# Performance work log

Measured on AMD Instinct MI355X. Metric: run time of the kernel, lower is better.

The kernel has to match this reference:

```python
import math
import jax, jax.numpy as jnp
import numpy as np

B = 64
INPUT_SIZE = 10080
PATCH = 18
S = INPUT_SIZE // PATCH  # 560 patches
E = 96                    # embed_dim
H = 12                    # num_heads
D = 96                    # head_dim == embed_dim (PAT quirk)
F = 256                   # ff_dim
L = 2                     # num_layers
EPS = 1e-5


def _sinusoidal_pe(seq_len, embed_dim):
    pos = jnp.arange(seq_len, dtype=jnp.float32)[:, None]
    div = jnp.exp(jnp.arange(0, embed_dim, 2, dtype=jnp.float32) * (-math.log(10000.0) / embed_dim))
    pe = jnp.zeros((seq_len, embed_dim), dtype=jnp.float32)
    pe = pe.at[:, 0::2].set(jnp.sin(pos * div))
    pe = pe.at[:, 1::2].set(jnp.cos(pos * div))
    return pe


def _layernorm(x, g, b):
    mu = jnp.mean(x, axis=-1, keepdims=True)
    var = jnp.var(x, axis=-1, keepdims=True)
    return (x - mu) * jax.lax.rsqrt(var + EPS) * g + b


def setup_inputs() -> dict:
    key = jax.random.key(0)
    ks = jax.random.split(key, 12)
    sd = 0.02
    inp = {
        "x": jax.random.normal(ks[0], (B, INPUT_SIZE), dtype=jnp.float32),
        "patch_W": jax.random.normal(ks[1], (PATCH, E), dtype=jnp.float32) * sd,
        "patch_b": jnp.zeros((E,), jnp.float32),
        "Wq": jax.random.normal(ks[2], (L, H, E, D), dtype=jnp.float32) * sd,
        "bq": jnp.zeros((L, H, D), jnp.float32),
        "Wk": jax.random.normal(ks[3], (L, H, E, D), dtype=jnp.float32) * sd,
        "bk": jnp.zeros((L, H, D), jnp.float32),
        "Wv": jax.random.normal(ks[4], (L, H, E, D), dtype=jnp.float32) * sd,
        "bv": jnp.zeros((L, H, D), jnp.float32),
        "Wo": jax.random.normal(ks[5], (L, H * D, E), dtype=jnp.float32) * sd,
        "bo": jnp.zeros((L, E), jnp.float32),
        "ff1_W": jax.random.normal(ks[6], (L, E, F), dtype=jnp.float32) * sd,
        "ff1_b": jnp.zeros((L, F), jnp.float32),
        "ff2_W": jax.random.normal(ks[7], (L, F, E), dtype=jnp.float32) * sd,
        "ff2_b": jnp.zeros((L, E), jnp.float32),
        "n1_g": jnp.ones((L, E), jnp.float32),
        "n1_b": jnp.zeros((L, E), jnp.float32),
        "n2_g": jnp.ones((L, E), jnp.float32),
        "n2_b": jnp.zeros((L, E), jnp.float32),
    }
    return inp


def reference(x, patch_W, patch_b, Wq, bq, Wk, bk, Wv, bv, Wo, bo,
              ff1_W, ff1_b, ff2_W, ff2_b, n1_g, n1_b, n2_g, n2_b):
    scale = 1.0 / math.sqrt(D)
    # patch embedding: [B, S, PATCH] -> [B, S, E]
    h = x.reshape(B, S, PATCH) @ patch_W + patch_b
    h = h + _sinusoidal_pe(S, E)[None]
    for l in range(L):
        # all heads at once (original loops over heads; same math)
        q = jnp.einsum('bse,hed->bhsd', h, Wq[l]) + bq[l][None, :, None, :]
        k = jnp.einsum('bse,hed->bhsd', h, Wk[l]) + bk[l][None, :, None, :]
        v = jnp.einsum('bse,hed->bhsd', h, Wv[l]) + bv[l][None, :, None, :]
        scores = jnp.einsum('bhsd,bhtd->bhst', q, k) * scale
        attn = jax.nn.softmax(scores, axis=-1)
        heads = jnp.einsum('bhst,bhtd->bhsd', attn, v)
        concat = heads.transpose(0, 2, 1, 3).reshape(B, S, H * D)
        attn_out = concat @ Wo[l] + bo[l]
        h = _layernorm(h + attn_out, n1_g[l], n1_b[l])
        ff = jax.nn.relu(h @ ff1_W[l] + ff1_b[l]) @ ff2_W[l] + ff2_b[l]
        h = _layernorm(h + ff, n2_g[l], n2_b[l])
    return h
```

## Files before the change

kernel.cpp:

```cpp
#include <hip/hip_runtime.h>
#include <hip/hip_bf16.h>
#include <math.h>

#define BATCH 64
#define CHUNK 32
#define INPUT_SIZE 10080
#define PATCH 18
#define SEQ 560
#define EMB 96
#define NHEAD 12
#define HDIM 96
#define FFDIM 256
#define NLAYER 2
#define TOK (BATCH * SEQ)
#define EPSV 1e-5f
#define SCALE 0.10206207261596577f

typedef __attribute__((ext_vector_type(8))) short bf16x8;
typedef __attribute__((ext_vector_type(4))) short bf16x4;
typedef __attribute__((ext_vector_type(4))) float f32x4;

static __device__ __forceinline__ short f2bf(float x) {
  union { __hip_bfloat16 b; short s; } u;
  u.b = __float2bfloat16(x);
  return u.s;
}

__global__ __launch_bounds__(256) void allprep_kernel(
    const float* __restrict__ Wq, const float* __restrict__ Wk,
    const float* __restrict__ Wv, const float* __restrict__ Wo,
    const float* __restrict__ ff1_W, const float* __restrict__ ff2_W,
    __hip_bfloat16* __restrict__ wqT, __hip_bfloat16* __restrict__ wkvT,
    __hip_bfloat16* __restrict__ woT, __hip_bfloat16* __restrict__ ff1WT,
    __hip_bfloat16* __restrict__ ff2WT) {
  int bx = blockIdx.x;
  if (bx < 72) {
    int hh = bx % NHEAD, mat = (bx / NHEAD) % 3, l = bx / 36;
    const float* src = (mat == 0 ? Wq : (mat == 1 ? Wk : Wv)) +
                       ((size_t)l * NHEAD + hh) * EMB * HDIM;
    __shared__ float t[HDIM * 97];
    for (int i = threadIdx.x; i < EMB * HDIM; i += 256) {
      int e = i / HDIM, d = i % HDIM;
      t[d * 97 + e] = src[i];
    }
    __syncthreads();
    __hip_bfloat16* dst;
    if (mat == 0)
      dst = wqT + ((size_t)l * NHEAD + hh) * HDIM * EMB;
    else
      dst = wkvT + ((size_t)l * 2 * NHEAD * HDIM + (mat - 1) * NHEAD * HDIM +
                    hh * HDIM) * EMB;
    for (int j = threadIdx.x; j < HDIM * EMB; j += 256) {
      int d = j / EMB, e = j % EMB;
      dst[j] = __float2bfloat16(t[d * 97 + e]);
    }
  } else if (bx < 74) {
    int l = bx - 72;
    const float* src = Wo + (size_t)l * NHEAD * HDIM * EMB;
    __hip_bfloat16* dst = woT + (size_t)l * EMB * NHEAD * HDIM;
    for (int i = threadIdx.x; i < EMB * NHEAD * HDIM; i += 256) {
      int e = i / (NHEAD * HDIM), j = i % (NHEAD * HDIM);
      dst[i] = __float2bfloat16(src[(size_t)j * EMB + e]);
    }
  } else {
    int idx = bx - 74;
    int mat = idx % 2, l = idx / 2;
    if (mat == 0) {
      const float* src = ff1_W + (size_t)l * EMB * FFDIM;
      __hip_bfloat16* dst = ff1WT + (size_t)l * FFDIM * EMB;
      for (int i = threadIdx.x; i < FFDIM * EMB; i += 256) {
        int f = i / EMB, e = i % EMB;
        dst[i] = __float2bfloat16(src[(size_t)e * FFDIM + f]);
      }
    } else {
      const float* src = ff2_W + (size_t)l * FFDIM * EMB;
      __hip_bfloat16* dst = ff2WT + (size_t)l * EMB * FFDIM;
      for (int i = threadIdx.x; i < EMB * FFDIM; i += 256) {
        int e = i / FFDIM, f = i % FFDIM;
        dst[i] = __float2bfloat16(src[(size_t)f * EMB + e]);
      }
    }
  }
}

__global__ void patch_pe_kernel(const float* __restrict__ x,
                                const float* __restrict__ W,
                                const float* __restrict__ bias,
                                float* __restrict__ h,
                                __hip_bfloat16* __restrict__ hbf) {
  int gid = blockIdx.x * blockDim.x + threadIdx.x;
  if (gid >= TOK * EMB) return;
  int tok = gid / EMB;
  int e = gid % EMB;
  int b = tok / SEQ;
  int s = tok % SEQ;
  const float* xp = x + b * INPUT_SIZE + s * PATCH;
  float acc = bias[e];
#pragma unroll
  for (int p = 0; p < PATCH; p++) acc += xp[p] * W[p * EMB + e];
  int i = e >> 1;
  float freq = __expf(-(float)(2 * i) * (9.210340371976184f / 96.0f));
  float ang = (float)s * freq;
  acc += (e & 1) ? cosf(ang) : sinf(ang);
  h[gid] = acc;
  hbf[gid] = __float2bfloat16(acc);
}

__global__ __launch_bounds__(256) void kv_mfma_kernel(
    const __hip_bfloat16* __restrict__ hbf,
    const __hip_bfloat16* __restrict__ wkvT, const float* __restrict__ bk,
    const float* __restrict__ bv, __hip_bfloat16* __restrict__ kbuf,
    __hip_bfloat16* __restrict__ vbufT, int b0) {
  const int wave = threadIdx.x >> 6;
  const int lane = threadIdx.x & 63;
  const int tq = lane & 15;
  const int quad = lane >> 4;
  const int m0 = blockIdx.x * 64 + wave * 16;
  const int n0 = blockIdx.y * 64;

  __shared__ short tile[4][16][68];

  const short* ap =
      (const short*)hbf + ((size_t)b0 * SEQ + m0 + tq) * EMB + quad * 8;
  bf16x8 a0 = *(const bf16x8*)(ap);
  bf16x8 a1 = *(const bf16x8*)(ap + 32);
  bf16x8 a2 = *(const bf16x8*)(ap + 64);

  f32x4 acc[4];
  const f32x4 zero4 = {0.f, 0.f, 0.f, 0.f};
#pragma unroll
  for (int nt = 0; nt < 4; nt++) acc[nt] = zero4;
#pragma unroll
  for (int nt = 0; nt < 4; nt++) {
    const short* bp =
        (const short*)wkvT + (size_t)(n0 + nt * 16 + tq) * EMB + quad * 8;
    bf16x8 b0f = *(const bf16x8*)(bp);
    bf16x8 b1f = *(const bf16x8*)(bp + 32);
    bf16x8 b2f = *(const bf16x8*)(bp + 64);
    acc[nt] = __builtin_amdgcn_mfma_f32_16x16x32_bf16(a0, b0f, acc[nt], 0, 0, 0);
    acc[nt] = __builtin_amdgcn_mfma_f32_16x16x32_bf16(a1, b1f, acc[nt], 0, 0, 0);
    acc[nt] = __builtin_amdgcn_mfma_f32_16x16x32_bf16(a2, b2f, acc[nt], 0, 0, 0);
  }

  const int tl0 = m0 + quad * 4;
  const int blb = tl0 / SEQ;
  const int ss0 = tl0 - blb * SEQ;

  if (n0 < NHEAD * HDIM) {
#pragma unroll
    for (int nt = 0; nt < 4; nt++) {
      int n = n0 + nt * 16 + tq;
      float bias = bk[n];
#pragma unroll
      for (int j = 0; j < 4; j++)
        tile[wave][quad * 4 + j][nt * 16 + tq] = f2bf(acc[nt][j] + bias);
    }
#pragma unroll
    for (int it = 0; it < 2; it++) {
      int idx = it * 64 + lane;
      int row = idx >> 3;
      int seg = idx & 7;
      int tl = m0 + row;
      int bb = tl / SEQ;
      int ss = tl - bb * SEQ;
      int r0s = n0 + seg * 8;
      int hh2 = r0s / HDIM;
      int d0 = r0s - hh2 * HDIM;
      bf16x8 v = *(const bf16x8*)&tile[wave][row][seg * 8];
      *(bf16x8*)((short*)kbuf +
                 ((size_t)(bb * NHEAD + hh2) * SEQ + ss) * HDIM + d0) = v;
    }
  } else {
#pragma unroll
    for (int nt = 0; nt < 4; nt++) {
      int n = n0 + nt * 16 + tq;
      int r = n - NHEAD * HDIM;
      int hh2 = r / HDIM;
      int d = r - hh2 * HDIM;
      float bias = bv[r];
      bf16x4 pack;
#pragma unroll
      for (int j = 0; j < 4; j++) pack[j] = f2bf(acc[nt][j] + bias);
      *(bf16x4*)((short*)vbufT +
                 ((size_t)(blb * NHEAD + hh2) * HDIM + d) * SEQ + ss0) = pack;
    }
  }
}

#define QW 104
#define PW 72
__global__ __launch_bounds__(256, 3) void attn_flash_kernel(
    const __hip_bfloat16* __restrict__ hbf,
    const __hip_bfloat16* __restrict__ wqT, const float* __restrict__ bq,
    const __hip_bfloat16* __restrict__ kbuf,
    const __hip_bfloat16* __restrict__ vbufT,
    __hip_bfloat16* __restrict__ heads, int b0) {
  const int flat = blockIdx.x;
  const int xcd = flat & 7;
  const int slot = flat >> 3;
  const int g = (slot / 5) * 8 + xcd;
  const int qt = slot % 5;
  const int hh = g % NHEAD;
  const int bl = g / NHEAD;
  const int wave = threadIdx.x >> 6;
  const int lane = threadIdx.x & 63;
  const int tq = lane & 15;
  const int quad = lane >> 4;

  __shared__ __align__(16) short sbuf[4][3328];
  short* pw = sbuf[wave];

  const size_t bh = (size_t)(bl * NHEAD + hh);
  const short* kb = (const short*)kbuf + bh * SEQ * HDIM;
  const short* vb = (const short*)vbufT + bh * HDIM * SEQ;

  const int q0 = qt * 128 + wave * 32;

  int qrA = q0 + tq;      if (qrA > SEQ - 1) qrA = SEQ - 1;
  int qrB = q0 + 16 + tq; if (qrB > SEQ - 1) qrB = SEQ - 1;
  const short* hpA =
      (const short*)hbf + ((size_t)(b0 + bl) * SEQ + qrA) * EMB + quad * 8;
  const short* hpB =
      (const short*)hbf + ((size_t)(b0 + bl) * SEQ + qrB) * EMB + quad * 8;
  bf16x8 haA0 = *(const bf16x8*)(hpA);
  bf16x8 haA1 = *(const bf16x8*)(hpA + 32);
  bf16x8 haA2 = *(const bf16x8*)(hpA + 64);
  bf16x8 haB0 = *(const bf16x8*)(hpB);
  bf16x8 haB1 = *(const bf16x8*)(hpB + 32);
  bf16x8 haB2 = *(const bf16x8*)(hpB + 64);
  const f32x4 zero4 = {0.f, 0.f, 0.f, 0.f};
  f32x4 qaccA[6], qaccB[6];
#pragma unroll
  for (int dt = 0; dt < 6; dt++) { qaccA[dt] = zero4; qaccB[dt] = zero4; }
#pragma unroll
  for (int dt = 0; dt < 6; dt++) {
    const short* wp = (const short*)wqT +
                      ((size_t)hh * HDIM + dt * 16 + tq) * EMB + quad * 8;
    bf16x8 w0 = *(const bf16x8*)(wp);
    bf16x8 w1 = *(const bf16x8*)(wp + 32);
    bf16x8 w2 = *(const bf16x8*)(wp + 64);
    qaccA[dt] = __builtin_amdgcn_mfma_f32_16x16x32_bf16(haA0, w0, qaccA[dt], 0, 0, 0);
    qaccA[dt] = __builtin_amdgcn_mfma_f32_16x16x32_bf16(haA1, w1, qaccA[dt], 0, 0, 0);
    qaccA[dt] = __builtin_amdgcn_mfma_f32_16x16x32_bf16(haA2, w2, qaccA[dt], 0, 0, 0);
    qaccB[dt] = __builtin_amdgcn_mfma_f32_16x16x32_bf16(haB0, w0, qaccB[dt], 0, 0, 0);
    qaccB[dt] = __builtin_amdgcn_mfma_f32_16x16x32_bf16(haB1, w1, qaccB[dt], 0, 0, 0);
    qaccB[dt] = __builtin_amdgcn_mfma_f32_16x16x32_bf16(haB2, w2, qaccB[dt], 0, 0, 0);
  }
#pragma unroll
  for (int dt = 0; dt < 6; dt++) {
    int d = dt * 16 + tq;
    float bias = bq[hh * HDIM + d];
#pragma unroll
    for (int r = 0; r < 4; r++) {
      pw[(quad * 4 + r) * QW + d] = f2bf((qaccA[dt][r] + bias) * SCALE);
      pw[(16 + quad * 4 + r) * QW + d] = f2bf((qaccB[dt][r] + bias) * SCALE);
    }
  }
  bf16x8 aqA0 = *(const bf16x8*)&pw[tq * QW + quad * 8];
  bf16x8 aqA1 = *(const bf16x8*)&pw[tq * QW + 32 + quad * 8];
  bf16x8 aqA2 = *(const bf16x8*)&pw[tq * QW + 64 + quad * 8];
  bf16x8 aqB0 = *(const bf16x8*)&pw[(16 + tq) * QW + quad * 8];
  bf16x8 aqB1 = *(const bf16x8*)&pw[(16 + tq) * QW + 32 + quad * 8];
  bf16x8 aqB2 = *(const bf16x8*)&pw[(16 + tq) * QW + 64 + quad * 8];

  f32x4 oA[6], oB[6];
#pragma unroll
  for (int dt = 0; dt < 6; dt++) { oA[dt] = zero4; oB[dt] = zero4; }
  float mA[4], mB[4], lA[4], lB[4];
#pragma unroll
  for (int r = 0; r < 4; r++) {
    mA[r] = -1e30f; mB[r] = -1e30f; lA[r] = 0.f; lB[r] = 0.f;
  }

  for (int c = 0; c < 9; c++) {
    const int col0 = c * 64;
    f32x4 sA[4], sB[4];
#pragma unroll
    for (int t = 0; t < 4; t++) { sA[t] = zero4; sB[t] = zero4; }
#pragma unroll
    for (int t = 0; t < 4; t++) {
      const short* kp = kb + (size_t)(col0 + t * 16 + tq) * HDIM + quad * 8;
      bf16x8 k0 = *(const bf16x8*)(kp);
      bf16x8 k1 = *(const bf16x8*)(kp + 32);
      bf16x8 k2 = *(const bf16x8*)(kp + 64);
      sA[t] = __builtin_amdgcn_mfma_f32_16x16x32_bf16(aqA0, k0, sA[t], 0, 0, 0);
      sA[t] = __builtin_amdgcn_mfma_f32_16x16x32_bf16(aqA1, k1, sA[t], 0, 0, 0);
      sA[t] = __builtin_amdgcn_mfma_f32_16x16x32_bf16(aqA2, k2, sA[t], 0, 0, 0);
      sB[t] = __builtin_amdgcn_mfma_f32_16x16x32_bf16(aqB0, k0, sB[t], 0, 0, 0);
      sB[t] = __builtin_amdgcn_mfma_f32_16x16x32_bf16(aqB1, k1, sB[t], 0, 0, 0);
      sB[t] = __builtin_amdgcn_mfma_f32_16x16x32_bf16(aqB2, k2, sB[t], 0, 0, 0);
    }
    if (c == 8) {
#pragma unroll
      for (int r = 0; r < 4; r++) { sA[3][r] = -1e30f; sB[3][r] = -1e30f; }
    }
    float cA[4], cB[4];
#pragma unroll
    for (int r = 0; r < 4; r++) {
      cA[r] = fmaxf(fmaxf(sA[0][r], sA[1][r]), fmaxf(sA[2][r], sA[3][r]));
      cB[r] = fmaxf(fmaxf(sB[0][r], sB[1][r]), fmaxf(sB[2][r], sB[3][r]));
    }
#pragma unroll
    for (int mask = 1; mask < 16; mask <<= 1) {
#pragma unroll
      for (int r = 0; r < 4; r++) {
        cA[r] = fmaxf(cA[r], __shfl_xor(cA[r], mask, 64));
        cB[r] = fmaxf(cB[r], __shfl_xor(cB[r], mask, 64));
      }
    }
    bool need = false;
#pragma unroll
    for (int r = 0; r < 4; r++)
      need = need | (cA[r] > mA[r]) | (cB[r] > mB[r]);
    if (__any(need)) {
#pragma unroll
      for (int r = 0; r < 4; r++) {
        float mnA = fmaxf(mA[r], cA[r]);
        float fA = __expf(mA[r] - mnA);
        mA[r] = mnA; lA[r] *= fA;
        float mnB = fmaxf(mB[r], cB[r]);
        float fB = __expf(mB[r] - mnB);
        mB[r] = mnB; lB[r] *= fB;
#pragma unroll
        for (int dt = 0; dt < 6; dt++) { oA[dt][r] *= fA; oB[dt][r] *= fB; }
      }
    }
#pragma unroll
    for (int t = 0; t < 4; t++) {
#pragma unroll
      for (int r = 0; r < 4; r++) {
        float pA = __expf(sA[t][r] - mA[r]);
        lA[r] += pA;
        pw[(quad * 4 + r) * PW + t * 16 + tq] = f2bf(pA);
        float pB = __expf(sB[t][r] - mB[r]);
        lB[r] += pB;
        pw[(16 + quad * 4 + r) * PW + t * 16 + tq] = f2bf(pB);
      }
    }
    bf16x8 paA0 = *(const bf16x8*)&pw[tq * PW + quad * 8];
    bf16x8 paA1 = *(const bf16x8*)&pw[tq * PW + 32 + quad * 8];
    bf16x8 paB0 = *(const bf16x8*)&pw[(16 + tq) * PW + quad * 8];
    bf16x8 paB1 = *(const bf16x8*)&pw[(16 + tq) * PW + 32 + quad * 8];
#pragma unroll
    for (int dt = 0; dt < 6; dt++) {
      const short* vp = vb + (size_t)(dt * 16 + tq) * SEQ + col0 + quad * 8;
      bf16x8 v0 = *(const bf16x8*)(vp);
      bf16x8 v1 = *(const bf16x8*)(vp + 32);
      oA[dt] = __builtin_amdgcn_mfma_f32_16x16x32_bf16(paA0, v0, oA[dt], 0, 0, 0);
      oA[dt] = __builtin_amdgcn_mfma_f32_16x16x32_bf16(paA1, v1, oA[dt], 0, 0, 0);
      oB[dt] = __builtin_amdgcn_mfma_f32_16x16x32_bf16(paB0, v0, oB[dt], 0, 0, 0);
      oB[dt] = __builtin_amdgcn_mfma_f32_16x16x32_bf16(paB1, v1, oB[dt], 0, 0, 0);
    }
  }

#pragma unroll
  for (int mask = 1; mask < 16; mask <<= 1) {
#pragma unroll
    for (int r = 0; r < 4; r++) {
      lA[r] += __shfl_xor(lA[r], mask, 64);
      lB[r] += __shfl_xor(lB[r], mask, 64);
    }
  }
  float rA[4], rB[4];
#pragma unroll
  for (int r = 0; r < 4; r++) { rA[r] = 1.f / lA[r]; rB[r] = 1.f / lB[r]; }
  __hip_bfloat16* hpout =
      heads + ((size_t)(b0 + bl) * SEQ) * (NHEAD * HDIM) + (size_t)hh * HDIM;
  const int qgA = q0 + quad * 4;
  const int qgB = q0 + 16 + quad * 4;
#pragma unroll
  for (int dt = 0; dt < 6; dt++) {
    int d = dt * 16 + tq;
#pragma unroll
    for (int r = 0; r < 4; r++) {
      if (qgA + r < SEQ)
        hpout[(size_t)(qgA + r) * (NHEAD * HDIM) + d] =
            __float2bfloat16(oA[dt][r] * rA[r]);
      if (qgB + r < SEQ)
        hpout[(size_t)(qgB + r) * (NHEAD * HDIM) + d] =
            __float2bfloat16(oB[dt][r] * rB[r]);
    }
  }
}

__global__ __launch_bounds__(256) void wo_ln_mfma_kernel(
    const __hip_bfloat16* __restrict__ heads,
    const __hip_bfloat16* __restrict__ woT, const float* __restrict__ bo,
    const float* __restrict__ gamma, const float* __restrict__ beta,
    const float* __restrict__ hres, float* __restrict__ hA,
    __hip_bfloat16* __restrict__ hbf) {
  const int wave = threadIdx.x >> 6;
  const int lane = threadIdx.x & 63;
  const int tq = lane & 15;
  const int quad = lane >> 4;
  const int m0 = blockIdx.x * 64 + wave * 16;

  const short* ap = (const short*)heads + (size_t)(m0 + tq) * (NHEAD * HDIM);
  const short* bp = (const short*)woT;

  f32x4 acc[6];
  const f32x4 zero4 = {0.f, 0.f, 0.f, 0.f};
#pragma unroll
  for (int dt = 0; dt < 6; dt++) acc[dt] = zero4;

  for (int kt = 0; kt < 36; kt++) {
    bf16x8 af = *(const bf16x8*)(ap + kt * 32 + quad * 8);
#pragma unroll
    for (int dt = 0; dt < 6; dt++) {
      bf16x8 bfr = *(const bf16x8*)(bp + (size_t)(dt * 16 + tq) * (NHEAD * HDIM) +
                                    kt * 32 + quad * 8);
      acc[dt] = __builtin_amdgcn_mfma_f32_16x16x32_bf16(af, bfr, acc[dt], 0, 0, 0);
    }
  }

  const int tok0 = m0 + quad * 4;
  float s1[4] = {0.f, 0.f, 0.f, 0.f};
  float s2[4] = {0.f, 0.f, 0.f, 0.f};
#pragma unroll
  for (int dt = 0; dt < 6; dt++) {
    int n = dt * 16 + tq;
    float bias = bo[n];
#pragma unroll
    for (int r = 0; r < 4; r++) {
      float val = acc[dt][r] + bias + hres[(size_t)(tok0 + r) * EMB + n];
      acc[dt][r] = val;
      s1[r] += val;
      s2[r] += val * val;
    }
  }
#pragma unroll
  for (int mask = 1; mask < 16; mask <<= 1) {
#pragma unroll
    for (int r = 0; r < 4; r++) {
      s1[r] += __shfl_xor(s1[r], mask, 64);
      s2[r] += __shfl_xor(s2[r], mask, 64);
    }
  }
  float mean[4], rstd[4];
#pragma unroll
  for (int r = 0; r < 4; r++) {
    mean[r] = s1[r] * (1.0f / EMB);
    float var = s2[r] * (1.0f / EMB) - mean[r] * mean[r];
    rstd[r] = rsqrtf(var + EPSV);
  }
#pragma unroll
  for (int dt = 0; dt < 6; dt++) {
    int n = dt * 16 + tq;
    float g = gamma[n], bt = beta[n];
#pragma unroll
    for (int r = 0; r < 4; r++) {
      float o = (acc[dt][r] - mean[r]) * rstd[r] * g + bt;
      hA[(size_t)(tok0 + r) * EMB + n] = o;
      hbf[(size_t)(tok0 + r) * EMB + n] = __float2bfloat16(o);
    }
  }
}

__global__ __launch_bounds__(256) void ff1_mfma_kernel(
    const __hip_bfloat16* __restrict__ hbf,
    const __hip_bfloat16* __restrict__ ff1WT, const float* __restrict__ b1,
    __hip_bfloat16* __restrict__ ffbf) {
  const int wave = threadIdx.x >> 6;
  const int lane = threadIdx.x & 63;
  const int tq = lane & 15;
  const int quad = lane >> 4;
  const int m0 = blockIdx.x * 64 + wave * 16;

  const short* ap = (const short*)hbf + (size_t)(m0 + tq) * EMB + quad * 8;
  bf16x8 a0 = *(const bf16x8*)(ap);
  bf16x8 a1 = *(const bf16x8*)(ap + 32);
  bf16x8 a2 = *(const bf16x8*)(ap + 64);

  f32x4 acc[16];
  const f32x4 zero4 = {0.f, 0.f, 0.f, 0.f};
#pragma unroll
  for (int nt = 0; nt < 16; nt++) acc[nt] = zero4;
#pragma unroll
  for (int nt = 0; nt < 16; nt++) {
    const short* bp =
        (const short*)ff1WT + (size_t)(nt * 16 + tq) * EMB + quad * 8;
    bf16x8 b0f = *(const bf16x8*)(bp);
    bf16x8 b1f = *(const bf16x8*)(bp + 32);
    bf16x8 b2f = *(const bf16x8*)(bp + 64);
    acc[nt] = __builtin_amdgcn_mfma_f32_16x16x32_bf16(a0, b0f, acc[nt], 0, 0, 0);
    acc[nt] = __builtin_amdgcn_mfma_f32_16x16x32_bf16(a1, b1f, acc[nt], 0, 0, 0);
    acc[nt] = __builtin_amdgcn_mfma_f32_16x16x32_bf16(a2, b2f, acc[nt], 0, 0, 0);
  }

  const int tok0 = m0 + quad * 4;
#pragma unroll
  for (int nt = 0; nt < 16; nt++) {
    int n = nt * 16 + tq;
    float bias = b1[n];
#pragma unroll
    for (int r = 0; r < 4; r++) {
      ffbf[(size_t)(tok0 + r) * FFDIM + n] =
          __float2bfloat16(fmaxf(acc[nt][r] + bias, 0.f));
    }
  }
}

__global__ __launch_bounds__(256) void ff2_ln_mfma_kernel(
    const __hip_bfloat16* __restrict__ ffbf,
    const __hip_bfloat16* __restrict__ ff2WT, const float* __restrict__ b2,
    const float* __restrict__ gamma, const float* __restrict__ beta,
    const float* __restrict__ hres, float* __restrict__ hout,
    __hip_bfloat16* __restrict__ hbf_out) {
  const int wave = threadIdx.x >> 6;
  const int lane = threadIdx.x & 63;
  const int tq = lane & 15;
  const int quad = lane >> 4;
  const int m0 = blockIdx.x * 64 + wave * 16;

  const short* ap = (const short*)ffbf + (size_t)(m0 + tq) * FFDIM;
  const short* bp = (const short*)ff2WT;

  f32x4 acc[6];
  const f32x4 zero4 = {0.f, 0.f, 0.f, 0.f};
#pragma unroll
  for (int dt = 0; dt < 6; dt++) acc[dt] = zero4;

#pragma unroll
  for (int kt = 0; kt < 8; kt++) {
    bf16x8 af = *(const bf16x8*)(ap + kt * 32 + quad * 8);
#pragma unroll
    for (int dt = 0; dt < 6; dt++) {
      bf16x8 bfr = *(const bf16x8*)(bp + (size_t)(dt * 16 + tq) * FFDIM +
                                    kt * 32 + quad * 8);
      acc[dt] = __builtin_amdgcn_mfma_f32_16x16x32_bf16(af, bfr, acc[dt], 0, 0, 0);
    }
  }

  const int tok0 = m0 + quad * 4;
  float s1[4] = {0.f, 0.f, 0.f, 0.f};
  float s2[4] = {0.f, 0.f, 0.f, 0.f};
#pragma unroll
  for (int dt = 0; dt < 6; dt++) {
    int n = dt * 16 + tq;
    float bias = b2[n];
#pragma unroll
    for (int r = 0; r < 4; r++) {
      float val = acc[dt][r] + bias + hres[(size_t)(tok0 + r) * EMB + n];
      acc[dt][r] = val;
      s1[r] += val;
      s2[r] += val * val;
    }
  }
#pragma unroll
  for (int mask = 1; mask < 16; mask <<= 1) {
#pragma unroll
    for (int r = 0; r < 4; r++) {
      s1[r] += __shfl_xor(s1[r], mask, 64);
      s2[r] += __shfl_xor(s2[r], mask, 64);
    }
  }
  float mean[4], rstd[4];
#pragma unroll
  for (int r = 0; r < 4; r++) {
    mean[r] = s1[r] * (1.0f / EMB);
    float var = s2[r] * (1.0f / EMB) - mean[r] * mean[r];
    rstd[r] = rsqrtf(var + EPSV);
  }
#pragma unroll
  for (int dt = 0; dt < 6; dt++) {
    int n = dt * 16 + tq;
    float g = gamma[n], bt = beta[n];
#pragma unroll
    for (int r = 0; r < 4; r++) {
      float o = (acc[dt][r] - mean[r]) * rstd[r] * g + bt;
      hout[(size_t)(tok0 + r) * EMB + n] = o;
      hbf_out[(size_t)(tok0 + r) * EMB + n] = __float2bfloat16(o);
    }
  }
}

extern "C" void kernel_launch(void* const* d_in, const int* in_sizes, int n_in,
                              void* d_out, int out_size, void* d_ws,
                              size_t ws_size, hipStream_t stream) {
  const float* x = (const float*)d_in[0];
  const float* patch_W = (const float*)d_in[1];
  const float* patch_b = (const float*)d_in[2];
  const float* Wq = (const float*)d_in[3];
  const float* bq = (const float*)d_in[4];
  const float* Wk = (const float*)d_in[5];
  const float* bk = (const float*)d_in[6];
  const float* Wv = (const float*)d_in[7];
  const float* bv = (const float*)d_in[8];
  const float* Wo = (const float*)d_in[9];
  const float* bo = (const float*)d_in[10];
  const float* ff1_W = (const float*)d_in[11];
  const float* ff1_b = (const float*)d_in[12];
  const float* ff2_W = (const float*)d_in[13];
  const float* ff2_b = (const float*)d_in[14];
  const float* n1_g = (const float*)d_in[15];
  const float* n1_b = (const float*)d_in[16];
  const float* n2_g = (const float*)d_in[17];
  const float* n2_b = (const float*)d_in[18];

  const size_t h_bytes = (size_t)TOK * EMB * sizeof(float);
  const size_t hbf_bytes = (size_t)TOK * EMB * 2;
  const size_t kv_bytes = (size_t)CHUNK * NHEAD * SEQ * HDIM * 2;
  const size_t heads_bytes = (size_t)TOK * NHEAD * HDIM * 2;
  const size_t wqT_bytes = (size_t)NLAYER * NHEAD * HDIM * EMB * 2;
  const size_t wkvT_bytes = 2 * wqT_bytes;
  const size_t woT_bytes = (size_t)NLAYER * EMB * NHEAD * HDIM * 2;
  const size_t ffw_bytes = (size_t)NLAYER * FFDIM * EMB * 2;
  char* ws = (char*)d_ws;
  size_t off = 0;
  float* h = (float*)(ws + off); off += h_bytes;
  float* hA = (float*)(ws + off); off += h_bytes;
  __hip_bfloat16* hbf = (__hip_bfloat16*)(ws + off); off += hbf_bytes;
  __hip_bfloat16* kbuf = (__hip_bfloat16*)(ws + off); off += kv_bytes;
  __hip_bfloat16* vbufT = (__hip_bfloat16*)(ws + off); off += kv_bytes;
  __hip_bfloat16* heads = (__hip_bfloat16*)(ws + off); off += heads_bytes;
  __hip_bfloat16* wqT = (__hip_bfloat16*)(ws + off); off += wqT_bytes;
  __hip_bfloat16* wkvT = (__hip_bfloat16*)(ws + off); off += wkvT_bytes;
  __hip_bfloat16* woT = (__hip_bfloat16*)(ws + off); off += woT_bytes;
  __hip_bfloat16* ff1WT = (__hip_bfloat16*)(ws + off); off += ffw_bytes;
  __hip_bfloat16* ff2WT = (__hip_bfloat16*)(ws + off); off += ffw_bytes;
  __hip_bfloat16* ffbf = (__hip_bfloat16*)kbuf;

  allprep_kernel<<<78, 256, 0, stream>>>(Wq, Wk, Wv, Wo, ff1_W, ff2_W, wqT,
                                         wkvT, woT, ff1WT, ff2WT);
  patch_pe_kernel<<<(TOK * EMB + 255) / 256, 256, 0, stream>>>(x, patch_W,
                                                               patch_b, h, hbf);

  for (int l = 0; l < NLAYER; l++) {
    const __hip_bfloat16* wqT_l = wqT + (size_t)l * NHEAD * HDIM * EMB;
    const __hip_bfloat16* wkvT_l = wkvT + (size_t)l * 2 * NHEAD * HDIM * EMB;
    const __hip_bfloat16* woT_l = woT + (size_t)l * EMB * NHEAD * HDIM;
    const __hip_bfloat16* ff1WT_l = ff1WT + (size_t)l * FFDIM * EMB;
    const __hip_bfloat16* ff2WT_l = ff2WT + (size_t)l * EMB * FFDIM;
    const float* bq_l = bq + (size_t)l * NHEAD * HDIM;
    const float* bk_l = bk + (size_t)l * NHEAD * HDIM;
    const float* bv_l = bv + (size_t)l * NHEAD * HDIM;
    const float* bo_l = bo + (size_t)l * EMB;

    for (int c = 0; c < BATCH / CHUNK; c++) {
      int b0 = c * CHUNK;
      kv_mfma_kernel<<<dim3(CHUNK * SEQ / 64, 2 * NHEAD * HDIM / 64), 256, 0,
                       stream>>>(hbf, wkvT_l, bk_l, bv_l, kbuf, vbufT, b0);
      attn_flash_kernel<<<5 * NHEAD * CHUNK, 256, 0, stream>>>(
          hbf, wqT_l, bq_l, kbuf, vbufT, heads, b0);
    }
    wo_ln_mfma_kernel<<<TOK / 64, 256, 0, stream>>>(
        heads, woT_l, bo_l, n1_g + l * EMB, n1_b + l * EMB, h, hA, hbf);
    ff1_mfma_kernel<<<TOK / 64, 256, 0, stream>>>(hbf, ff1WT_l,
                                                  ff1_b + l * FFDIM, ffbf);
    float* dst = (l == NLAYER - 1) ? (float*)d_out : h;
    ff2_ln_mfma_kernel<<<TOK / 64, 256, 0, stream>>>(
        ffbf, ff2WT_l, ff2_b + l * EMB, n2_g + l * EMB, n2_b + l * EMB, hA,
        dst, hbf);
  }
}
```

Before: 1.251 ms.

## Transpose attention MFMA operands so each lane owns one query row

Swaps the MFMA A/B operands in the QK^T and PV products so score and output accumulators are laid out with one query per lane. Row max and row sum then reduce in registers plus two cross-quad shuffles instead of four-step shuffles over 16 lanes. The softmax is moved to base-2 by folding log2(e) into the Q scale and calling raw v_exp_f32. P is written to LDS as packed bf16 pairs and the output as bf16x4 vector stores. The occupancy hint is raised from 3 to 4 blocks per CU, which may force register spills.

```diff
diff --git a/kernel.cpp b/kernel.cpp
--- a/kernel.cpp
+++ b/kernel.cpp
@@ -15,15 +15,29 @@
 #define TOK (BATCH * SEQ)
 #define EPSV 1e-5f
 #define SCALE 0.10206207261596577f
+#define SCALE_L2E 0.14724443805513492f
 
 typedef __attribute__((ext_vector_type(8))) short bf16x8;
 typedef __attribute__((ext_vector_type(4))) short bf16x4;
 typedef __attribute__((ext_vector_type(4))) float f32x4;
+typedef __attribute__((ext_vector_type(2))) unsigned int u32x2;
 
 static __device__ __forceinline__ short f2bf(float x) {
   union { __hip_bfloat16 b; short s; } u;
   u.b = __float2bfloat16(x);
   return u.s;
+}
+
+static __device__ __forceinline__ unsigned int pack2bf(float lo, float hi) {
+  unsigned int a = (unsigned short)f2bf(lo);
+  unsigned int b = (unsigned short)f2bf(hi);
+  return a | (b << 16);
+}
+
+static __device__ __forceinline__ float exp2_fast(float x) {
+  float r;
+  asm("v_exp_f32 %0, %1" : "=v"(r) : "v"(x));
+  return r;
 }
 
 __global__ __launch_bounds__(256) void allprep_kernel(
@@ -188,8 +202,8 @@
 }
 
 #define QW 104
-#define PW 72
-__global__ __launch_bounds__(256, 3) void attn_flash_kernel(
+#define PW32 36
+__global__ __launch_bounds__(256, 4) void attn_flash_kernel(
     const __hip_bfloat16* __restrict__ hbf,
     const __hip_bfloat16* __restrict__ wqT, const float* __restrict__ bq,
     const __hip_bfloat16* __restrict__ kbuf,
@@ -209,6 +223,8 @@
 
   __shared__ __align__(16) short sbuf[4][3328];
   short* pw = sbuf[wave];
+  unsigned int* pwA = (unsigned int*)pw;
+  unsigned int* pwB = pwA + 16 * PW32;
 
   const size_t bh = (size_t)(bl * NHEAD + hh);
   const short* kb = (const short*)kbuf + bh * SEQ * HDIM;
@@ -252,8 +268,8 @@
     float bias = bq[hh * HDIM + d];
 #pragma unroll
     for (int r = 0; r < 4; r++) {
-      pw[(quad * 4 + r) * QW + d] = f2bf((qaccA[dt][r] + bias) * SCALE);
-      pw[(16 + quad * 4 + r) * QW + d] = f2bf((qaccB[dt][r] + bias) * SCALE);
+      pw[(quad * 4 + r) * QW + d] = f2bf((qaccA[dt][r] + bias) * SCALE_L2E);
+      pw[(16 + quad * 4 + r) * QW + d] = f2bf((qaccB[dt][r] + bias) * SCALE_L2E);
     }
   }
   bf16x8 aqA0 = *(const bf16x8*)&pw[tq * QW + quad * 8];
@@ -266,11 +282,7 @@
   f32x4 oA[6], oB[6];
 #pragma unroll
   for (int dt = 0; dt < 6; dt++) { oA[dt] = zero4; oB[dt] = zero4; }
-  float mA[4], mB[4], lA[4], lB[4];
-#pragma unroll
-  for (int r = 0; r < 4; r++) {
-    mA[r] = -1e30f; mB[r] = -1e30f; lA[r] = 0.f; lB[r] = 0.f;
-  }
+  float mA = -1e30f, mB = -1e30f, lA = 0.f, lB = 0.f;
 
   for (int c = 0; c < 9; c++) {
     const int col0 = c * 64;
@@ -283,102 +295,99 @@
       bf16x8 k0 = *(const bf16x8*)(kp);
       bf16x8 k1 = *(const bf16x8*)(kp + 32);
       bf16x8 k2 = *(const bf16x8*)(kp + 64);
-      sA[t] = __builtin_amdgcn_mfma_f32_16x16x32_bf16(aqA0, k0, sA[t], 0, 0, 0);
-      sA[t] = __builtin_amdgcn_mfma_f32_16x16x32_bf16(aqA1, k1, sA[t], 0, 0, 0);
-      sA[t] = __builtin_amdgcn_mfma_f32_16x16x32_bf16(aqA2, k2, sA[t], 0, 0, 0);
-      sB[t] = __builtin_amdgcn_mfma_f32_16x16x32_bf16(aqB0, k0, sB[t], 0, 0, 0);
-      sB[t] = __builtin_amdgcn_mfma_f32_16x16x32_bf16(aqB1, k1, sB[t], 0, 0, 0);
-      sB[t] = __builtin_amdgcn_mfma_f32_16x16x32_bf16(aqB2, k2, sB[t], 0, 0, 0);
+      sA[t] = __builtin_amdgcn_mfma_f32_16x16x32_bf16(k0, aqA0, sA[t], 0, 0, 0);
+      sA[t] = __builtin_amdgcn_mfma_f32_16x16x32_bf16(k1, aqA1, sA[t], 0, 0, 0);
+      sA[t] = __builtin_amdgcn_mfma_f32_16x16x32_bf16(k2, aqA2, sA[t], 0, 0, 0);
+      sB[t] = __builtin_amdgcn_mfma_f32_16x16x32_bf16(k0, aqB0, sB[t], 0, 0, 0);
+      sB[t] = __builtin_amdgcn_mfma_f32_16x16x32_bf16(k1, aqB1, sB[t], 0, 0, 0);
+      sB[t] = __builtin_amdgcn_mfma_f32_16x16x32_bf16(k2, aqB2, sB[t], 0, 0, 0);
     }
     if (c == 8) {
 #pragma unroll
       for (int r = 0; r < 4; r++) { sA[3][r] = -1e30f; sB[3][r] = -1e30f; }
     }
-    float cA[4], cB[4];
-#pragma unroll
-    for (int r = 0; r < 4; r++) {
-      cA[r] = fmaxf(fmaxf(sA[0][r], sA[1][r]), fmaxf(sA[2][r], sA[3][r]));
-      cB[r] = fmaxf(fmaxf(sB[0][r], sB[1][r]), fmaxf(sB[2][r], sB[3][r]));
-    }
-#pragma unroll
-    for (int mask = 1; mask < 16; mask <<= 1) {
+    float cA = sA[0][0], cB = sB[0][0];
+#pragma unroll
+    for (int t = 0; t < 4; t++) {
 #pragma unroll
       for (int r = 0; r < 4; r++) {
-        cA[r] = fmaxf(cA[r], __shfl_xor(cA[r], mask, 64));
-        cB[r] = fmaxf(cB[r], __shfl_xor(cB[r], mask, 64));
+        cA = fmaxf(cA, sA[t][r]);
+        cB = fmaxf(cB, sB[t][r]);
       }
     }
-    bool need = false;
-#pragma unroll
-    for (int r = 0; r < 4; r++)
-      need = need | (cA[r] > mA[r]) | (cB[r] > mB[r]);
-    if (__any(need)) {
-#pragma unroll
-      for (int r = 0; r < 4; r++) {
-        float mnA = fmaxf(mA[r], cA[r]);
-        float fA = __expf(mA[r] - mnA);
-        mA[r] = mnA; lA[r] *= fA;
-        float mnB = fmaxf(mB[r], cB[r]);
-        float fB = __expf(mB[r] - mnB);
-        mB[r] = mnB; lB[r] *= fB;
-#pragma unroll
-        for (int dt = 0; dt < 6; dt++) { oA[dt][r] *= fA; oB[dt][r] *= fB; }
+    cA = fmaxf(cA, __shfl_xor(cA, 16, 64));
+    cA = fmaxf(cA, __shfl_xor(cA, 32, 64));
+    cB = fmaxf(cB, __shfl_xor(cB, 16, 64));
+    cB = fmaxf(cB, __shfl_xor(cB, 32, 64));
+    if (__any((cA > mA) | (cB > mB))) {
+      float mnA = fmaxf(mA, cA);
+      float fA = exp2_fast(mA - mnA);
+      mA = mnA; lA *= fA;
+      float mnB = fmaxf(mB, cB);
+      float fB = exp2_fast(mB - mnB);
+      mB = mnB; lB *= fB;
+#pragma unroll
+      for (int dt = 0; dt < 6; dt++) {
+#pragma unroll
+        for (int r = 0; r < 4; r++) { oA[dt][r] *= fA; oB[dt][r] *= fB; }
       }
     }
 #pragma unroll
     for (int t = 0; t < 4; t++) {
-#pragma unroll
-      for (int r = 0; r < 4; r++) {
-        float pA = __expf(sA[t][r] - mA[r]);
-        lA[r] += pA;
-        pw[(quad * 4 + r) * PW + t * 16 + tq] = f2bf(pA);
-        float pB = __expf(sB[t][r] - mB[r]);
-        lB[r] += pB;
-        pw[(16 + quad * 4 + r) * PW + t * 16 + tq] = f2bf(pB);
-      }
-    }
-    bf16x8 paA0 = *(const bf16x8*)&pw[tq * PW + quad * 8];
-    bf16x8 paA1 = *(const bf16x8*)&pw[tq * PW + 32 + quad * 8];
-    bf16x8 paB0 = *(const bf16x8*)&pw[(16 + tq) * PW + quad * 8];
-    bf16x8 paB1 = *(const bf16x8*)&pw[(16 + tq) * PW + 32 + quad * 8];
+      float pA0 = exp2_fast(sA[t][0] - mA);
+      float pA1 = exp2_fast(sA[t][1] - mA);
+      float pA2 = exp2_fast(sA[t][2] - mA);
+      float pA3 = exp2_fast(sA[t][3] - mA);
+      lA += (pA0 + pA1) + (pA2 + pA3);
+      u32x2 wA = {pack2bf(pA0, pA1), pack2bf(pA2, pA3)};
+      *(u32x2*)&pwA[tq * PW32 + t * 8 + quad * 2] = wA;
+      float pB0 = exp2_fast(sB[t][0] - mB);
+      float pB1 = exp2_fast(sB[t][1] - mB);
+      float pB2 = exp2_fast(sB[t][2] - mB);
+      float pB3 = exp2_fast(sB[t][3] - mB);
+      lB += (pB0 + pB1) + (pB2 + pB3);
+      u32x2 wB = {pack2bf(pB0, pB1), pack2bf(pB2, pB3)};
+      *(u32x2*)&pwB[tq * PW32 + t * 8 + quad * 2] = wB;
+    }
+    bf16x8 paA0 = *(const bf16x8*)&pwA[tq * PW32 + quad * 4];
+    bf16x8 paA1 = *(const bf16x8*)&pwA[tq * PW32 + 16 + quad * 4];
+    bf16x8 paB0 = *(const bf16x8*)&pwB[tq * PW32 + quad * 4];
+    bf16x8 paB1 = *(const bf16x8*)&pwB[tq * PW32 + 16 + quad * 4];
 #pragma unroll
     for (int dt = 0; dt < 6; dt++) {
       const short* vp = vb + (size_t)(dt * 16 + tq) * SEQ + col0 + quad * 8;
       bf16x8 v0 = *(const bf16x8*)(vp);
       bf16x8 v1 = *(const bf16x8*)(vp + 32);
-      oA[dt] = __builtin_amdgcn_mfma_f32_16x16x32_bf16(paA0, v0, oA[dt], 0, 0, 0);
-      oA[dt] = __builtin_amdgcn_mfma_f32_16x16x32_bf16(paA1, v1, oA[dt], 0, 0, 0);
-      oB[dt] = __builtin_amdgcn_mfma_f32_16x16x32_bf16(paB0, v0, oB[dt], 0, 0, 0);
-      oB[dt] = __builtin_amdgcn_mfma_f32_16x16x32_bf16(paB1, v1, oB[dt], 0, 0, 0);
-    }
-  }
-
-#pragma unroll
-  for (int mask = 1; mask < 16; mask <<= 1) {
-#pragma unroll
-    for (int r = 0; r < 4; r++) {
-      lA[r] += __shfl_xor(lA[r], mask, 64);
-      lB[r] += __shfl_xor(lB[r], mask, 64);
-    }
-  }
-  float rA[4], rB[4];
-#pragma unroll
-  for (int r = 0; r < 4; r++) { rA[r] = 1.f / lA[r]; rB[r] = 1.f / lB[r]; }
-  __hip_bfloat16* hpout =
-      heads + ((size_t)(b0 + bl) * SEQ) * (NHEAD * HDIM) + (size_t)hh * HDIM;
-  const int qgA = q0 + quad * 4;
-  const int qgB = q0 + 16 + quad * 4;
+      oA[dt] = __builtin_amdgcn_mfma_f32_16x16x32_bf16(v0, paA0, oA[dt], 0, 0, 0);
+      oA[dt] = __builtin_amdgcn_mfma_f32_16x16x32_bf16(v1, paA1, oA[dt], 0, 0, 0);
+      oB[dt] = __builtin_amdgcn_mfma_f32_16x16x32_bf16(v0, paB0, oB[dt], 0, 0, 0);
+      oB[dt] = __builtin_amdgcn_mfma_f32_16x16x32_bf16(v1, paB1, oB[dt], 0, 0, 0);
+    }
+  }
+
+  lA += __shfl_xor(lA, 16, 64);
+  lA += __shfl_xor(lA, 32, 64);
+  lB += __shfl_xor(lB, 16, 64);
+  lB += __shfl_xor(lB, 32, 64);
+  float rA = 1.f / lA, rB = 1.f / lB;
+  short* hpout =
+      (short*)heads + ((size_t)(b0 + bl) * SEQ) * (NHEAD * HDIM) + hh * HDIM;
+  const int tokA = q0 + tq;
+  const int tokB = q0 + 16 + tq;
 #pragma unroll
   for (int dt = 0; dt < 6; dt++) {
-    int d = dt * 16 + tq;
-#pragma unroll
-    for (int r = 0; r < 4; r++) {
-      if (qgA + r < SEQ)
-        hpout[(size_t)(qgA + r) * (NHEAD * HDIM) + d] =
-            __float2bfloat16(oA[dt][r] * rA[r]);
-      if (qgB + r < SEQ)
-        hpout[(size_t)(qgB + r) * (NHEAD * HDIM) + d] =
-            __float2bfloat16(oB[dt][r] * rB[r]);
+    int d0 = dt * 16 + quad * 4;
+    if (tokA < SEQ) {
+      bf16x4 pk;
+#pragma unroll
+      for (int r = 0; r < 4; r++) pk[r] = f2bf(oA[dt][r] * rA);
+      *(bf16x4*)(hpout + (size_t)tokA * (NHEAD * HDIM) + d0) = pk;
+    }
+    if (tokB < SEQ) {
+      bf16x4 pk;
+#pragma unroll
+      for (int r = 0; r < 4; r++) pk[r] = f2bf(oB[dt][r] * rB);
+      *(bf16x4*)(hpout + (size_t)tokB * (NHEAD * HDIM) + d0) = pk;
     }
   }
 }
```

After: 1.431 ms. 14.3% more time.
